# Kernel tuning notes

Measured on AMD Instinct MI355X. Metric: run time of the kernel, lower is better.

Reference implementation:

```python
import jax, jax.numpy as jnp
import numpy as np

S = 7  # output_size


def _bin_indices(lo, hi, dim):
    """PyTorch AdaptiveMaxPool windows for each of S bins over [lo, hi] (inclusive).
    Returns gather indices [R,S,K] and validity mask [R,S,K].
    start_i = floor(i*L/S), end_i = ceil((i+1)*L/S), L = hi-lo+1."""
    L = hi - lo + 1  # [R]
    i = jnp.arange(S)
    start = lo[:, None] + (i * L[:, None]) // S          # [R,S]
    end = lo[:, None] + ((i + 1) * L[:, None] + S - 1) // S  # [R,S]
    K = (dim + S - 1) // S + 1  # static max window size
    k = jnp.arange(K)
    idx = start[:, :, None] + k                          # [R,S,K]
    valid = idx < end[:, :, None]
    return jnp.clip(idx, 0, dim - 1), valid


def setup_inputs() -> dict:
    key = jax.random.key(0)
    k1, k2 = jax.random.split(key)
    feature_map = jax.random.normal(k1, (1, 256, 64, 64), dtype=jnp.float32)
    # generate valid ROIs: sort coordinate pairs so x1<=x2, y1<=y2
    pairs = jax.random.randint(k2, (1, 128, 2, 2), 0, 64)  # [B,R,(x|y),2]
    pairs = jnp.sort(pairs, axis=-1)
    rois = jnp.stack(
        [pairs[..., 0, 0], pairs[..., 1, 0], pairs[..., 0, 1], pairs[..., 1, 1]],
        axis=-1,
    ).astype(jnp.int32)  # [1,128,4] = (x1,y1,x2,y2)
    return {"feature_map": feature_map, "rois": rois}


def reference(feature_map, rois):
    f = feature_map[0]  # [C,H,W]  (module only works with batch=1)
    C, H, W = f.shape
    r = rois.reshape(-1, 4).astype(jnp.int32)
    x1, y1, x2, y2 = r[:, 0], r[:, 1], r[:, 2], r[:, 3]
    neg = jnp.finfo(f.dtype).min

    # pool over dim 2 (x / f_wid axis, per original slicing feature_map[:,:,x1:x2+1,...])
    h_idx, h_val = _bin_indices(x1, x2, H)               # [R,S,Kh]
    g1 = f[:, h_idx, :]                                  # [C,R,S,Kh,W]
    rowmax = jnp.max(jnp.where(h_val[None, :, :, :, None], g1, neg), axis=3)  # [C,R,S,W]

    # pool over dim 3 (y / f_hei axis)
    w_idx, w_val = _bin_indices(y1, y2, W)               # [R,S,Kw]
    R_, Sw, Kw = w_idx.shape
    g2 = jnp.take_along_axis(rowmax, w_idx.reshape(1, R_, 1, Sw * Kw), axis=3)
    g2 = g2.reshape(C, R_, S, Sw, Kw)                    # [C,R,S,S,Kw]
    pooled = jnp.max(jnp.where(w_val[None, :, None, :, :], g2, neg), axis=4)  # [C,R,S,S]

    # pooled_rois[b, roi, c, S, S] -> flatten to [1, R, C, S*S]
    out = pooled.transpose(1, 0, 2, 3).reshape(1, R_, C, S * S)
    return out
```

## Files before the change

### kernel.cpp

```cpp
#include <hip/hip_runtime.h>
#include <cfloat>

#define NS 7
#define NC 256
#define NH 64
#define NW 64
#define NR 128

__global__ __launch_bounds__(256) void roi_pool_kernel(
    const float* __restrict__ f,
    const int* __restrict__ rois,
    float* __restrict__ out)
{
    __shared__ float colmax_lds[4][NS][NW];

    const int lane = threadIdx.x & 63;
    const int wid  = threadIdx.x >> 6;

    const int r  = blockIdx.x >> 6;
    const int cg = blockIdx.x & 63;
    const int c  = cg * 4 + wid;

    const int x1 = rois[4 * r + 0];
    const int y1 = rois[4 * r + 1];
    const int x2 = rois[4 * r + 2];
    const int y2 = rois[4 * r + 3];
    const int Lh = x2 - x1 + 1;
    const int Lw = y2 - y1 + 1;

    const float* fc = f + (size_t)c * (NH * NW);

    for (int i = 0; i < NS; ++i) {
        const int hs = x1 + (i * Lh) / NS;
        const int he = x1 + ((i + 1) * Lh + NS - 1) / NS;
        float m = -FLT_MAX;
        if (lane < Lw) {
            const float* p = fc + hs * NW + y1 + lane;
            for (int h = hs; h < he; ++h) {
                m = fmaxf(m, *p);
                p += NW;
            }
        }
        colmax_lds[wid][i][lane] = m;
    }

    __syncthreads();

    if (lane < NS * NS) {
        const int i  = lane / NS;
        const int j  = lane % NS;
        const int cs = (j * Lw) / NS;
        const int ce = ((j + 1) * Lw + NS - 1) / NS;
        float m = -FLT_MAX;
        #pragma unroll 1
        for (int k = cs; k < ce; ++k)
            m = fmaxf(m, colmax_lds[wid][i][k]);
        out[((size_t)(r * NC + c)) * (NS * NS) + lane] = m;
    }
}

extern "C" void kernel_launch(void* const* d_in, const int* in_sizes, int n_in,
                              void* d_out, int out_size, void* d_ws, size_t ws_size,
                              hipStream_t stream)
{
    const float* feature_map = (const float*)d_in[0];
    const int*   rois        = (const int*)d_in[1];
    float*       out         = (float*)d_out;

    const int grid  = NR * (NC / 4);
    const int block = 256;

    roi_pool_kernel<<<grid, block, 0, stream>>>(feature_map, rois, out);
}
```

Baseline: 28.01 us.

## Stage full channel plane in LDS and pool 32 ROIs per block

Switches the work split from one block per (ROI, 4 channels) to one block per (channel, group of 32 ROIs). Each block loads the whole 64x64 channel plane into padded shared memory with float4 loads, precomputes the bin bounds for its ROIs, and each thread computes one output bin by a direct 2D max over LDS. This targets the repeated global reads of the same channel data across ROIs. The cost is 2D loops per bin with uneven trip counts, which cause divergence and heavier LDS traffic, and output writes that are scattered.

```diff
diff --git a/kernel.cpp b/kernel.cpp
--- a/kernel.cpp
+++ b/kernel.cpp
@@ -6,56 +6,68 @@
 #define NH 64
 #define NW 64
 #define NR 128
+#define RG 32
+#define LDW 68
 
 __global__ __launch_bounds__(256) void roi_pool_kernel(
     const float* __restrict__ f,
     const int* __restrict__ rois,
     float* __restrict__ out)
 {
-    __shared__ float colmax_lds[4][NS][NW];
+    __shared__ float plane[NH * LDW];
+    __shared__ int hs[RG][NS], he[RG][NS];
+    __shared__ int ws[RG][NS], we[RG][NS];
 
-    const int lane = threadIdx.x & 63;
-    const int wid  = threadIdx.x >> 6;
+    const int tid = threadIdx.x;
+    const int c   = blockIdx.x >> 2;
+    const int g   = blockIdx.x & 3;
 
-    const int r  = blockIdx.x >> 6;
-    const int cg = blockIdx.x & 63;
-    const int c  = cg * 4 + wid;
+    {
+        const float4* src = (const float4*)(f + (size_t)c * (NH * NW));
+        #pragma unroll
+        for (int k = 0; k < 4; ++k) {
+            int q  = tid + k * 256;
+            int h  = q >> 4;
+            int w4 = q & 15;
+            float4 v = src[q];
+            *(float4*)&plane[h * LDW + w4 * 4] = v;
+        }
+    }
 
-    const int x1 = rois[4 * r + 0];
-    const int y1 = rois[4 * r + 1];
-    const int x2 = rois[4 * r + 2];
-    const int y2 = rois[4 * r + 3];
-    const int Lh = x2 - x1 + 1;
-    const int Lw = y2 - y1 + 1;
-
-    const float* fc = f + (size_t)c * (NH * NW);
-
-    for (int i = 0; i < NS; ++i) {
-        const int hs = x1 + (i * Lh) / NS;
-        const int he = x1 + ((i + 1) * Lh + NS - 1) / NS;
-        float m = -FLT_MAX;
-        if (lane < Lw) {
-            const float* p = fc + hs * NW + y1 + lane;
-            for (int h = hs; h < he; ++h) {
-                m = fmaxf(m, *p);
-                p += NW;
-            }
+    if (tid < RG) {
+        int r  = g * RG + tid;
+        int x1 = rois[4*r+0], y1 = rois[4*r+1];
+        int x2 = rois[4*r+2], y2 = rois[4*r+3];
+        int Lh = x2 - x1 + 1, Lw = y2 - y1 + 1;
+        #pragma unroll
+        for (int i = 0; i < NS; ++i) {
+            hs[tid][i] = x1 + (i * Lh) / NS;
+            he[tid][i] = x1 + ((i + 1) * Lh + NS - 1) / NS;
+            ws[tid][i] = y1 + (i * Lw) / NS;
+            we[tid][i] = y1 + ((i + 1) * Lw + NS - 1) / NS;
         }
-        colmax_lds[wid][i][lane] = m;
     }
 
     __syncthreads();
 
-    if (lane < NS * NS) {
-        const int i  = lane / NS;
-        const int j  = lane % NS;
-        const int cs = (j * Lw) / NS;
-        const int ce = ((j + 1) * Lw + NS - 1) / NS;
+    for (int o = tid; o < RG * NS * NS; o += 256) {
+        int lr  = o / (NS * NS);
+        int bin = o - lr * (NS * NS);
+        int i   = bin / NS;
+        int j   = bin - i * NS;
+
+        int h0 = hs[lr][i], h1 = he[lr][i];
+        int w0 = ws[lr][j], w1 = we[lr][j];
+
         float m = -FLT_MAX;
-        #pragma unroll 1
-        for (int k = cs; k < ce; ++k)
-            m = fmaxf(m, colmax_lds[wid][i][k]);
-        out[((size_t)(r * NC + c)) * (NS * NS) + lane] = m;
+        for (int h = h0; h < h1; ++h) {
+            const float* row = &plane[h * LDW];
+            for (int w = w0; w < w1; ++w)
+                m = fmaxf(m, row[w]);
+        }
+
+        int r = g * RG + lr;
+        out[((size_t)(r * NC + c)) * (NS * NS) + bin] = m;
     }
 }
 
@@ -67,7 +79,7 @@
     const int*   rois        = (const int*)d_in[1];
     float*       out         = (float*)d_out;
 
-    const int grid  = NR * (NC / 4);
+    const int grid  = NC * (NR / RG);
     const int block = 256;
 
     roi_pool_kernel<<<grid, block, 0, stream>>>(feature_map, rois, out);
```

Result: slower. 35.47 us (+26.6%).

## Transpose feature map to HWC and pool per-bin with channel-coalesced loads

Applied to the files above, without the earlier changes.

Adds a pre-pass kernel that transposes the CHW feature map into an HWC workspace, so the pooling kernel can have each lane handle one channel and read contiguous channels for every (h,w) in a bin. The pooling kernel now computes each 7x7 bin directly over its 2D window, without the separate row-then-column reduction. Results are staged in LDS so the output is written with coalesced stores. The cost is an extra kernel launch, a full read and write of the feature map, and some redundant reads when adjacent bins overlap.

```diff
diff --git a/kernel.cpp b/kernel.cpp
--- a/kernel.cpp
+++ b/kernel.cpp
@@ -7,19 +7,39 @@
 #define NW 64
 #define NR 128
 
-__global__ __launch_bounds__(256) void roi_pool_kernel(
-    const float* __restrict__ f,
-    const int* __restrict__ rois,
+__global__ __launch_bounds__(256) void transpose_chw_hwc(
+    const float* __restrict__ f, float* __restrict__ ft)
+{
+    __shared__ float tile[64][65];
+    const int tid = threadIdx.x;
+    const int h   = blockIdx.x >> 2;
+    const int c0  = (blockIdx.x & 3) * 64;
+
+    #pragma unroll
+    for (int k = 0; k < 16; ++k) {
+        int q = tid + k * 256;
+        int c = q >> 6;
+        int w = q & 63;
+        tile[w][c] = f[(size_t)(c0 + c) * (NH * NW) + h * NW + w];
+    }
+    __syncthreads();
+    #pragma unroll
+    for (int k = 0; k < 16; ++k) {
+        int q = tid + k * 256;
+        int w = q >> 6;
+        int c = q & 63;
+        ft[(size_t)h * (NW * NC) + w * NC + c0 + c] = tile[w][c];
+    }
+}
+
+__global__ __launch_bounds__(512) void roi_pool_hwc(
+    const float* __restrict__ ft, const int* __restrict__ rois,
     float* __restrict__ out)
 {
-    __shared__ float colmax_lds[4][NS][NW];
-
-    const int lane = threadIdx.x & 63;
-    const int wid  = threadIdx.x >> 6;
-
-    const int r  = blockIdx.x >> 6;
-    const int cg = blockIdx.x & 63;
-    const int c  = cg * 4 + wid;
+    __shared__ float res[64 * NS * NS];
+    const int tid = threadIdx.x;
+    const int r   = blockIdx.x >> 2;
+    const int c0  = (blockIdx.x & 3) * 64;
 
     const int x1 = rois[4 * r + 0];
     const int y1 = rois[4 * r + 1];
@@ -28,35 +48,33 @@
     const int Lh = x2 - x1 + 1;
     const int Lw = y2 - y1 + 1;
 
-    const float* fc = f + (size_t)c * (NH * NW);
+    for (int o = tid; o < 64 * NS * NS; o += 512) {
+        int bin = __builtin_amdgcn_readfirstlane(o >> 6);
+        int c   = o & 63;
+        int i   = bin / NS;
+        int j   = bin % NS;
 
-    for (int i = 0; i < NS; ++i) {
-        const int hs = x1 + (i * Lh) / NS;
-        const int he = x1 + ((i + 1) * Lh + NS - 1) / NS;
+        int h0 = x1 + (i * Lh) / NS;
+        int h1 = x1 + ((i + 1) * Lh + NS - 1) / NS;
+        int w0 = y1 + (j * Lw) / NS;
+        int w1 = y1 + ((j + 1) * Lw + NS - 1) / NS;
+
         float m = -FLT_MAX;
-        if (lane < Lw) {
-            const float* p = fc + hs * NW + y1 + lane;
-            for (int h = hs; h < he; ++h) {
+        for (int h = h0; h < h1; ++h) {
+            const float* p = ft + ((size_t)(h * NW + w0)) * NC + c0 + c;
+            for (int w = w0; w < w1; ++w) {
                 m = fmaxf(m, *p);
-                p += NW;
+                p += NC;
             }
         }
-        colmax_lds[wid][i][lane] = m;
+        res[c * (NS * NS) + bin] = m;
     }
 
     __syncthreads();
 
-    if (lane < NS * NS) {
-        const int i  = lane / NS;
-        const int j  = lane % NS;
-        const int cs = (j * Lw) / NS;
-        const int ce = ((j + 1) * Lw + NS - 1) / NS;
-        float m = -FLT_MAX;
-        #pragma unroll 1
-        for (int k = cs; k < ce; ++k)
-            m = fmaxf(m, colmax_lds[wid][i][k]);
-        out[((size_t)(r * NC + c)) * (NS * NS) + lane] = m;
-    }
+    const size_t base = ((size_t)r * NC + c0) * (NS * NS);
+    for (int t = tid; t < 64 * NS * NS; t += 512)
+        out[base + t] = res[t];
 }
 
 extern "C" void kernel_launch(void* const* d_in, const int* in_sizes, int n_in,
@@ -66,9 +84,8 @@
     const float* feature_map = (const float*)d_in[0];
     const int*   rois        = (const int*)d_in[1];
     float*       out         = (float*)d_out;
+    float*       ft          = (float*)d_ws;
 
-    const int grid  = NR * (NC / 4);
-    const int block = 256;
-
-    roi_pool_kernel<<<grid, block, 0, stream>>>(feature_map, rois, out);
+    transpose_chw_hwc<<<NH * 4, 256, 0, stream>>>(feature_map, ft);
+    roi_pool_hwc<<<NR * 4, 512, 0, stream>>>(ft, rois, out);
 }
```

New measurement: 56.33 us. 2.01x slower.

## Process four ROIs per block with float2 loads and permlane half-wave reduction

Applied to the files above, without the earlier changes.

Each block now handles four ROIs for four channels, looping over the ROIs so the channel plane is reused from cache. Each wave reads two rows at once, one per 32-lane half, using float2 loads. The halves are combined with v_permlane32_swap, and results go to a per-wave LDS stripe without a block-wide barrier. The second-stage window max is a fixed six-step unrolled loop with masks. The aim is fewer idle lanes, fewer serial row iterations and fewer blocks, at the cost of more registers and less parallelism per block. The fixed six-pair loop assumes a window span of at most twelve columns.

```diff
diff --git a/kernel.cpp b/kernel.cpp
--- a/kernel.cpp
+++ b/kernel.cpp
@@ -6,56 +6,105 @@
 #define NH 64
 #define NW 64
 #define NR 128
+#define SW 76
 
 __global__ __launch_bounds__(256) void roi_pool_kernel(
     const float* __restrict__ f,
     const int* __restrict__ rois,
     float* __restrict__ out)
 {
-    __shared__ float colmax_lds[4][NS][NW];
+    __shared__ float stripe_all[4][NS][SW];
 
-    const int lane = threadIdx.x & 63;
-    const int wid  = threadIdx.x >> 6;
+    const int tid  = threadIdx.x;
+    const int lane = tid & 63;
+    const int wid  = tid >> 6;
+    float (*stripe)[SW] = stripe_all[wid];
 
-    const int r  = blockIdx.x >> 6;
-    const int cg = blockIdx.x & 63;
-    const int c  = cg * 4 + wid;
-
-    const int x1 = rois[4 * r + 0];
-    const int y1 = rois[4 * r + 1];
-    const int x2 = rois[4 * r + 2];
-    const int y2 = rois[4 * r + 3];
-    const int Lh = x2 - x1 + 1;
-    const int Lw = y2 - y1 + 1;
+    const int cq = blockIdx.x >> 5;
+    const int g  = blockIdx.x & 31;
+    const int c  = cq * 4 + wid;
 
     const float* fc = f + (size_t)c * (NH * NW);
+    const int l31  = lane & 63 & 31;
+    const int half = lane >> 5;
 
-    for (int i = 0; i < NS; ++i) {
-        const int hs = x1 + (i * Lh) / NS;
-        const int he = x1 + ((i + 1) * Lh + NS - 1) / NS;
-        float m = -FLT_MAX;
-        if (lane < Lw) {
-            const float* p = fc + hs * NW + y1 + lane;
-            for (int h = hs; h < he; ++h) {
-                m = fmaxf(m, *p);
-                p += NW;
+    const int bl = lane < NS * NS ? lane : NS * NS - 1;
+    const int bi = bl / NS;
+    const int bj = bl - bi * NS;
+
+    for (int rr = 0; rr < 4; ++rr) {
+        const int r  = g * 4 + rr;
+        const int x1 = rois[4*r+0], y1 = rois[4*r+1];
+        const int x2 = rois[4*r+2], y2 = rois[4*r+3];
+        const unsigned Lh = (unsigned)(x2 - x1 + 1);
+        const unsigned Lw = (unsigned)(y2 - y1 + 1);
+
+        const int d0    = y1 >> 1;
+        const int dspan = (y2 >> 1) - d0 + 1;
+        const bool wact = (l31 < dspan);
+        const int  dcl  = d0 + (wact ? l31 : dspan - 1);
+
+        int hs[NS], he[NS];
+        #pragma unroll
+        for (int i = 0; i < NS; ++i) {
+            hs[i] = x1 + (int)((unsigned)(i * Lh) / NS);
+            he[i] = x1 + (int)(((unsigned)((i + 1) * Lh) + NS - 1) / NS);
+        }
+
+        float2 acc[NS];
+        #pragma unroll
+        for (int i = 0; i < NS; ++i) {
+            int row  = hs[i] + half;
+            bool v   = wact && (row < he[i]);
+            int rowc = v ? row : hs[i];
+            float2 t = *(const float2*)(fc + rowc * NW + dcl * 2);
+            acc[i].x = v ? t.x : -FLT_MAX;
+            acc[i].y = v ? t.y : -FLT_MAX;
+        }
+        int mp = (int)(((Lh + NS - 1) / NS + 2) >> 1);
+        for (int k = 1; k < mp; ++k) {
+            #pragma unroll
+            for (int i = 0; i < NS; ++i) {
+                int row0 = hs[i] + 2 * k;
+                if (row0 < he[i]) {
+                    int row  = row0 + half;
+                    bool v   = wact && (row < he[i]);
+                    int rowc = v ? row : row0;
+                    float2 t = *(const float2*)(fc + rowc * NW + dcl * 2);
+                    acc[i].x = fmaxf(acc[i].x, v ? t.x : -FLT_MAX);
+                    acc[i].y = fmaxf(acc[i].y, v ? t.y : -FLT_MAX);
+                }
             }
         }
-        colmax_lds[wid][i][lane] = m;
-    }
 
-    __syncthreads();
+        #pragma unroll
+        for (int i = 0; i < NS; ++i) {
+            float ax = acc[i].x, bx = acc[i].x;
+            float ay = acc[i].y, by = acc[i].y;
+            asm("v_permlane32_swap_b32 %0, %1" : "+v"(ax), "+v"(bx));
+            asm("v_permlane32_swap_b32 %0, %1" : "+v"(ay), "+v"(by));
+            float mx = fmaxf(ax, bx);
+            float my = fmaxf(ay, by);
+            if (half == 0 && wact) {
+                *(float2*)&stripe[i][2 * dcl] = make_float2(mx, my);
+            }
+        }
 
-    if (lane < NS * NS) {
-        const int i  = lane / NS;
-        const int j  = lane % NS;
-        const int cs = (j * Lw) / NS;
-        const int ce = ((j + 1) * Lw + NS - 1) / NS;
-        float m = -FLT_MAX;
-        #pragma unroll 1
-        for (int k = cs; k < ce; ++k)
-            m = fmaxf(m, colmax_lds[wid][i][k]);
-        out[((size_t)(r * NC + c)) * (NS * NS) + lane] = m;
+        {
+            int wsj = y1 + (int)((unsigned)(bj * Lw) / NS);
+            int wej = y1 + (int)(((unsigned)((bj + 1) * Lw) + NS - 1) / NS);
+            int base2 = wsj & ~1;
+            float m = -FLT_MAX;
+            #pragma unroll
+            for (int k = 0; k < 6; ++k) {
+                float2 v = *(const float2*)&stripe[bi][base2 + 2 * k];
+                int w0 = base2 + 2 * k;
+                m = fmaxf(m, (w0     >= wsj && w0     < wej) ? v.x : -FLT_MAX);
+                m = fmaxf(m, (w0 + 1 < wej)                  ? v.y : -FLT_MAX);
+            }
+            if (lane < NS * NS)
+                out[((size_t)r * NC + c) * (NS * NS) + lane] = m;
+        }
     }
 }
 
@@ -67,7 +116,7 @@
     const int*   rois        = (const int*)d_in[1];
     float*       out         = (float*)d_out;
 
-    const int grid  = NR * (NC / 4);
+    const int grid  = 64 * 32;
     const int block = 256;
 
     roi_pool_kernel<<<grid, block, 0, stream>>>(feature_map, rois, out);
```

Measured after the change: 42.46 us. +51.6%, slower.
